# Performance work log

Hardware: AMD Instinct MI355X
Metric: run time of the kernel (lower is better)

Reference implementation:

```python
import jax, jax.numpy as jnp
import numpy as np

ROPE_THETA = 10000.0


def _apply_rope(x, rot_dim):
    # lucidrains RotaryEmbedding: only first rot_dim channels are rotated,
    # freqs are interleave-repeated, rotate_half works on (d r=2) pairs.
    S = x.shape[-2]
    half = rot_dim // 2
    inv_freq = 1.0 / (ROPE_THETA ** (jnp.arange(0, rot_dim, 2, dtype=jnp.float32) / rot_dim))  # [half]
    pos = jnp.arange(S, dtype=jnp.float32)
    freqs = pos[:, None] * inv_freq[None, :]          # [S, half]
    freqs = jnp.repeat(freqs, 2, axis=-1)             # [S, rot_dim] interleaved
    cos = jnp.cos(freqs).astype(x.dtype)
    sin = jnp.sin(freqs).astype(x.dtype)
    xl, xr = x[..., :rot_dim], x[..., rot_dim:]
    xp = xl.reshape(*xl.shape[:-1], half, 2)
    x1, x2 = xp[..., 0], xp[..., 1]
    rot_half = jnp.stack([-x2, x1], axis=-1).reshape(xl.shape)
    return jnp.concatenate([xl * cos + rot_half * sin, xr], axis=-1)


def setup_inputs() -> dict:
    key = jax.random.key(0)
    ks = jax.random.split(key, 7)
    B, Sa, Se, d_audio, d_score = 4, 4096, 2048, 1024, 1024
    d_h = min(d_audio, d_score)
    return {
        "x_audio": jax.random.normal(ks[0], (B, Sa, d_audio), jnp.float32),
        "x_event": jax.random.normal(ks[1], (B, Se, d_score), jnp.float32),
        "event_padding_mask": jax.random.randint(ks[2], (B, Se), 0, 2) > 0,
        "W_q": jax.random.normal(ks[3], (d_h, d_audio), jnp.float32) * (d_audio ** -0.5),
        "b_q": jax.random.normal(ks[4], (d_h,), jnp.float32) * 0.02,
        "W_k": jax.random.normal(ks[5], (d_h, d_score), jnp.float32) * (d_score ** -0.5),
        "b_k": jax.random.normal(ks[6], (d_h,), jnp.float32) * 0.02,
    }


def reference(x_audio, x_event, event_padding_mask, W_q, b_q, W_k, b_k):
    d_h = W_q.shape[0]
    rot_dim = d_h // 2  # RotaryEmbedding(dim=d_h//2) -> partial rotary over first d_h//2 channels
    Q = jnp.einsum("bsd,hd->bsh", x_audio, W_q) + b_q
    K = jnp.einsum("bed,hd->beh", x_event, W_k) + b_k
    Q = _apply_rope(Q, rot_dim)
    K = _apply_rope(K, rot_dim)
    attn = jnp.einsum("bsh,beh->bse", Q, K)  # [B, S_audio, S_event]
    mask = event_padding_mask[:, None, :]     # [B, 1, S_event]
    attn = jnp.where(mask, attn, jnp.float32(-jnp.inf))
    return attn
```

## Files before the change

### kernel.cpp

```cpp
#include <hip/hip_runtime.h>
#include <hip/hip_bf16.h>
#include <cmath>

#define BATCH 4
#define SA 4096
#define SE 2048
#define DIM 1024
#define ROT 512
#define NT (DIM / 64)

#define MASK_SENTINEL (-1.0e30f)

using short8  = __attribute__((ext_vector_type(8))) short;
using floatx4 = __attribute__((ext_vector_type(4))) float;

#define RFREQ 0.0519051171f

__device__ __forceinline__ void gl_lds16(const void* g, void* l) {
    __builtin_amdgcn_global_load_lds(
        (const __attribute__((address_space(1))) unsigned int*)g,
        (__attribute__((address_space(3))) unsigned int*)l, 16, 0, 0);
}

__device__ __forceinline__ short bf16_of(float f) {
    __hip_bfloat16 h = __float2bfloat16(f);
    return *reinterpret_cast<short*>(&h);
}

__device__ __forceinline__ int imin(int a, int b) { return a < b ? a : b; }

__global__ __launch_bounds__(256) void probe_mask_kernel(
    const int* __restrict__ mask_i, int* __restrict__ flag)
{
    __shared__ int s_bad;
    if (threadIdx.x == 0) s_bad = 0;
    __syncthreads();
    int bad = 0;
    for (int i = threadIdx.x; i < 1024; i += 256) {
        int v = mask_i[i];
        bad |= (v != 0 && v != 1) ? 1 : 0;
    }
    if (bad) atomicOr(&s_bad, 1);
    __syncthreads();
    if (threadIdx.x == 0) *flag = s_bad ? 0 : 1;
}

__global__ __launch_bounds__(256) void cvt_bf16_kernel(
    const float* __restrict__ in, short* __restrict__ out, int n8)
{
    int i = blockIdx.x * 256 + threadIdx.x;
    if (i >= n8) return;
    const float4 f0 = ((const float4*)in)[2 * i];
    const float4 f1 = ((const float4*)in)[2 * i + 1];
    short8 o;
    o[0] = bf16_of(f0.x); o[1] = bf16_of(f0.y);
    o[2] = bf16_of(f0.z); o[3] = bf16_of(f0.w);
    o[4] = bf16_of(f1.x); o[5] = bf16_of(f1.y);
    o[6] = bf16_of(f1.z); o[7] = bf16_of(f1.w);
    ((short8*)out)[i] = o;
}

__global__ __launch_bounds__(256) void rope_table_kernel(float2* __restrict__ tab)
{
    const int i   = blockIdx.x * 256 + threadIdx.x;
    const int h2  = i >> 12;
    const int pos = i & 4095;
    const float inv = exp2f(-RFREQ * (float)h2);
    float s, c;
    sincosf((float)pos * inv, &s, &c);
    tab[i] = make_float2(c, s);
}

template <int MODE>
__device__ __forceinline__ void gemm128_body(
    const short* __restrict__ A,
    const short* __restrict__ B,
    const float* __restrict__ bias,
    const float2* __restrict__ ct,
    const void*  __restrict__ maskp,
    const int*   __restrict__ flag,
    void* __restrict__ outp,
    int smask)
{
    __shared__ char smem[65536];
    char* const lA0 = smem;
    char* const lA1 = smem + 16384;
    char* const lB0 = smem + 32768;
    char* const lB1 = smem + 49152;

    const int tid  = threadIdx.x;
    const int wid  = tid >> 6;
    const int lane = tid & 63;

    const int nbx = gridDim.x, nby = gridDim.y;
    const int id  = blockIdx.x + nbx * (blockIdx.y + nby * blockIdx.z);
    const int cpx = (nbx * nby * gridDim.z) >> 3;
    const int swzid = (id & 7) * cpx + (id >> 3);
    const int bx  = swzid % nbx;
    const int byz = swzid / nbx;
    const int by  = byz % nby;
    const int bz  = byz / nby;
    const int m0 = by * 128;
    const int n0 = bx * 128;

    const short* Ab = A;
    const short* Bb = B;
    if (MODE == 1) {
        Ab += (size_t)bz * SA * DIM;
        Bb += (size_t)bz * SE * DIM;
    }

    const int r8   = lane >> 3;
    const int c16  = (lane & 7) << 4;
    const int scs  = ((lane & 7) ^ r8) << 4;
    const int arow = wid * 8 + r8;
    const char* gA = (const char*)Ab + ((size_t)(m0 + arow) << 11) + scs;
    const char* gB = (const char*)Bb + ((size_t)(n0 + arow) << 11) + scs;
    const int ldsT = arow * 128 + c16;

#define STG_A(dst, j, kt) \
    gl_lds16(gA + (((size_t)(j) * 32) << 11) + (size_t)(kt) * 128, \
             (dst) + (j) * 32 * 128 + ldsT)
#define STG_B(dst, j, kt) \
    gl_lds16(gB + (((size_t)(j) * 32) << 11) + (size_t)(kt) * 128, \
             (dst) + (j) * 32 * 128 + ldsT)

    const int fr  = lane & 15;
    const int fq  = lane >> 4;
    const int kc0 = (fq * 16) ^ ((fr & 7) << 4);
    const int wm  = (wid >> 1) * 64;
    const int wn  = (wid & 1) * 64;

    floatx4 acc[4][4] = {};
    short8 af[4][2];
    short8 b01[2][2];
    short8 b23[2][2];

#define RD_A(lAc) do {                                                       \
    _Pragma("unroll") for (int mi = 0; mi < 4; ++mi)                         \
    _Pragma("unroll") for (int ks = 0; ks < 2; ++ks)                         \
        af[mi][ks] = *(const short8*)((lAc)                                  \
            + (wm + mi * 16 + fr) * 128 + (kc0 ^ (ks * 64)));                \
} while (0)
#define RD_B01(lBc) do {                                                     \
    _Pragma("unroll") for (int ni = 0; ni < 2; ++ni)                         \
    _Pragma("unroll") for (int ks = 0; ks < 2; ++ks)                         \
        b01[ni][ks] = *(const short8*)((lBc)                                 \
            + (wn + ni * 16 + fr) * 128 + (kc0 ^ (ks * 64)));                \
} while (0)
#define RD_B23(lBc) do {                                                     \
    _Pragma("unroll") for (int ni = 0; ni < 2; ++ni)                         \
    _Pragma("unroll") for (int ks = 0; ks < 2; ++ks)                         \
        b23[ni][ks] = *(const short8*)((lBc)                                 \
            + (wn + (2 + ni) * 16 + fr) * 128 + (kc0 ^ (ks * 64)));          \
} while (0)
#define QUAD01() do {                                                        \
    __builtin_amdgcn_s_setprio(1);                                           \
    _Pragma("unroll") for (int mi = 0; mi < 4; ++mi)                         \
    _Pragma("unroll") for (int ni = 0; ni < 2; ++ni)                         \
    _Pragma("unroll") for (int ks = 0; ks < 2; ++ks)                         \
        acc[mi][ni] = __builtin_amdgcn_mfma_f32_16x16x32_bf16(               \
            af[mi][ks], b01[ni][ks], acc[mi][ni], 0, 0, 0);                  \
    __builtin_amdgcn_s_setprio(0);                                           \
} while (0)
#define QUAD23() do {                                                        \
    __builtin_amdgcn_s_setprio(1);                                           \
    _Pragma("unroll") for (int mi = 0; mi < 4; ++mi)                         \
    _Pragma("unroll") for (int ni = 0; ni < 2; ++ni)                         \
    _Pragma("unroll") for (int ks = 0; ks < 2; ++ks)                         \
        acc[mi][2 + ni] = __builtin_amdgcn_mfma_f32_16x16x32_bf16(           \
            af[mi][ks], b23[ni][ks], acc[mi][2 + ni], 0, 0, 0);              \
    __builtin_amdgcn_s_setprio(0);                                           \
} while (0)
#define BAR() do { __builtin_amdgcn_s_barrier();                             \
                   __builtin_amdgcn_sched_barrier(0); } while (0)
#define WAITV(n) asm volatile("s_waitcnt vmcnt(" #n ")" ::: "memory")

    STG_A(lA0, 0, 0); STG_A(lA0, 1, 0); STG_A(lA0, 2, 0); STG_A(lA0, 3, 0);
    STG_B(lB0, 0, 0); STG_B(lB0, 1, 0); STG_B(lB0, 2, 0); STG_B(lB0, 3, 0);
    STG_A(lA1, 0, 1); STG_A(lA1, 1, 1); STG_A(lA1, 2, 1); STG_A(lA1, 3, 1);
    WAITV(4);
    BAR();

    auto tile = [&](int t, char* lAc, char* lBc, char* lBo) {
        const int kt1 = imin(t + 1, NT - 1);
        const int kt2 = imin(t + 2, NT - 1);
        RD_A(lAc); RD_B01(lBc);
        STG_B(lBo, 0, kt1); STG_B(lBo, 1, kt1);
        STG_B(lBo, 2, kt1); STG_B(lBo, 3, kt1);
        BAR();
        QUAD01();
        BAR();
        RD_B23(lBc);
        STG_A(lAc, 0, kt2); STG_A(lAc, 1, kt2);
        STG_A(lAc, 2, kt2); STG_A(lAc, 3, kt2);
        BAR();
        QUAD23();
        WAITV(4);
        BAR();
    };

    for (int t = 0; t < NT; t += 2) {
        tile(t,     lA0, lB0, lB1);
        tile(t + 1, lA1, lB1, lB0);
    }
    WAITV(0);

    const int rrow = fq * 4;

    if (MODE == 0) {
        short* out = (short*)outp;
#pragma unroll
        for (int ni = 0; ni < 4; ++ni) {
            const int h = n0 + wn + ni * 16 + fr;
            const float bv  = bias[h];
            const bool rope = (h < ROT);
            const float sgn = (h & 1) ? 1.f : -1.f;
            const float2* ctrow = ct + ((size_t)(h >> 1) << 12);
#pragma unroll
            for (int mi = 0; mi < 4; ++mi) {
                const int rbase = m0 + wm + mi * 16 + rrow;
                const int pbase = rbase & smask;
                float2 cs[4];
                if (rope) {
#pragma unroll
                    for (int r = 0; r < 4; ++r) cs[r] = ctrow[pbase + r];
                }
#pragma unroll
                for (int r = 0; r < 4; ++r) {
                    float v = acc[mi][ni][r] + bv;
                    float p = __shfl_xor(v, 1);
                    if (rope) v = v * cs[r].x + sgn * p * cs[r].y;
                    out[(size_t)(rbase + r) * DIM + h] = bf16_of(v);
                }
            }
        }
    } else {
        float* out = (float*)outp + (size_t)bz * SA * SE;
        const int fl = *flag;
#pragma unroll
        for (int ni = 0; ni < 4; ++ni) {
            const int e = n0 + wn + ni * 16 + fr;
            int mk;
            if (fl) mk = ((const int*)maskp)[(size_t)bz * SE + e];
            else    mk = ((const unsigned char*)maskp)[(size_t)bz * SE + e];
#pragma unroll
            for (int mi = 0; mi < 4; ++mi) {
                const int rbase = m0 + wm + mi * 16 + rrow;
#pragma unroll
                for (int r = 0; r < 4; ++r) {
                    const float v = mk ? acc[mi][ni][r] : MASK_SENTINEL;
                    out[(size_t)(rbase + r) * SE + e] = v;
                }
            }
        }
    }
#undef STG_A
#undef STG_B
#undef RD_A
#undef RD_B01
#undef RD_B23
#undef QUAD01
#undef QUAD23
#undef BAR
#undef WAITV
}

__global__ __launch_bounds__(256, 2) void gemm128_proj_kernel(
    const short* __restrict__ A, const short* __restrict__ B,
    const float* __restrict__ bias, const float2* __restrict__ ct,
    short* __restrict__ out, int smask)
{
    gemm128_body<0>(A, B, bias, ct, nullptr, nullptr, out, smask);
}

__global__ __launch_bounds__(256, 2) void gemm128_attn_kernel(
    const short* __restrict__ Q, const short* __restrict__ K,
    const void* __restrict__ maskp, const int* __restrict__ flag,
    float* __restrict__ out)
{
    gemm128_body<1>(Q, K, nullptr, nullptr, maskp, flag, out, 0);
}

extern "C" void kernel_launch(void* const* d_in, const int* in_sizes, int n_in,
                              void* d_out, int out_size, void* d_ws, size_t ws_size,
                              hipStream_t stream)
{
    const float* x_audio = (const float*)d_in[0];
    const float* x_event = (const float*)d_in[1];
    const void*  maskp   = d_in[2];
    const float* W_q     = (const float*)d_in[3];
    const float* b_q     = (const float*)d_in[4];
    const float* W_k     = (const float*)d_in[5];
    const float* b_k     = (const float*)d_in[6];
    float* out = (float*)d_out;

    char* ws = (char*)d_ws;
    short* xbf  = (short*)(ws);
    short* Qbf  = (short*)(ws + (size_t)32 * 1024 * 1024);
    short* Kbf  = (short*)(ws + (size_t)64 * 1024 * 1024);
    short* Wqbf = (short*)(ws + (size_t)80 * 1024 * 1024);
    short* Wkbf = (short*)(ws + (size_t)82 * 1024 * 1024);
    int*   flag = (int*)  (ws + (size_t)84 * 1024 * 1024);
    float2* ct  = (float2*)d_out;

    probe_mask_kernel<<<1, 256, 0, stream>>>((const int*)maskp, flag);
    rope_table_kernel<<<4096, 256, 0, stream>>>(ct);

    const int nxa8 = BATCH * SA * DIM / 8;
    const int nxe8 = BATCH * SE * DIM / 8;
    const int nw8  = DIM * DIM / 8;

    cvt_bf16_kernel<<<(nxa8 + 255) / 256, 256, 0, stream>>>(x_audio, xbf, nxa8);
    cvt_bf16_kernel<<<(nw8 + 255) / 256, 256, 0, stream>>>(W_q, Wqbf, nw8);
    gemm128_proj_kernel<<<dim3(DIM / 128, (BATCH * SA) / 128, 1), 256, 0, stream>>>(
        xbf, Wqbf, b_q, ct, Qbf, SA - 1);

    cvt_bf16_kernel<<<(nxe8 + 255) / 256, 256, 0, stream>>>(x_event, xbf, nxe8);
    cvt_bf16_kernel<<<(nw8 + 255) / 256, 256, 0, stream>>>(W_k, Wkbf, nw8);
    gemm128_proj_kernel<<<dim3(DIM / 128, (BATCH * SE) / 128, 1), 256, 0, stream>>>(
        xbf, Wkbf, b_k, ct, Kbf, SE - 1);

    gemm128_attn_kernel<<<dim3(SE / 128, SA / 128, BATCH), 256, 0, stream>>>(
        Qbf, Kbf, maskp, flag, out);
}
```

Before: 374.7 us.

## Use 256x256 tiles with 512 threads and BK=32 for the attention GEMM

Replaces the shared 128x128 templated GEMM for the QK^T score computation with a dedicated kernel. It uses 256x256 output tiles, 8 waves, a K-step of 32 and a new LDS swizzle, while keeping the split-B double-buffered global_load_lds pipeline. Larger tiles halve global/L2 traffic per output element and raise MFMA work per LDS byte. In exchange each thread holds a 128-float accumulator, which adds register pressure and lowers occupancy, and the grid shrinks to 512 blocks. The projection GEMM is split out unchanged.

Result: slower. 991.9 us (+164.7%).

```diff
diff --git a/kernel.cpp b/kernel.cpp
--- a/kernel.cpp
+++ b/kernel.cpp
@@ -7,7 +7,14 @@
 #define SE 2048
 #define DIM 1024
 #define ROT 512
-#define NT (DIM / 64)
+
+#define BM 128
+#define BN 128
+#define BK 64
+#define NT (DIM / BK)
+
+#define ABK 32
+#define ANT (DIM / ABK)
 
 #define MASK_SENTINEL (-1.0e30f)
 
@@ -28,6 +35,10 @@
 }
 
 __device__ __forceinline__ int imin(int a, int b) { return a < b ? a : b; }
+
+#define BAR() do { __builtin_amdgcn_s_barrier();                             \
+                   __builtin_amdgcn_sched_barrier(0); } while (0)
+#define WAITV(n) asm volatile("s_waitcnt vmcnt(" #n ")" ::: "memory")
 
 __global__ __launch_bounds__(256) void probe_mask_kernel(
     const int* __restrict__ mask_i, int* __restrict__ flag)
@@ -71,16 +82,22 @@
     tab[i] = make_float2(c, s);
 }
 
-template <int MODE>
-__device__ __forceinline__ void gemm128_body(
-    const short* __restrict__ A,
-    const short* __restrict__ B,
-    const float* __restrict__ bias,
-    const float2* __restrict__ ct,
-    const void*  __restrict__ maskp,
-    const int*   __restrict__ flag,
-    void* __restrict__ outp,
-    int smask)
+__device__ __forceinline__ void xcd_swizzle(int& bx, int& by, int& bz)
+{
+    const int nbx = gridDim.x, nby = gridDim.y;
+    const int id  = blockIdx.x + nbx * (blockIdx.y + nby * blockIdx.z);
+    const int cpx = (nbx * nby * gridDim.z) >> 3;
+    const int swzid = (id & 7) * cpx + (id >> 3);
+    bx = swzid % nbx;
+    const int byz = swzid / nbx;
+    by = byz % nby;
+    bz = byz / nby;
+}
+
+__global__ __launch_bounds__(256, 2) void gemm_proj_kernel(
+    const short* __restrict__ A, const short* __restrict__ B,
+    const float* __restrict__ bias, const float2* __restrict__ ct,
+    short* __restrict__ out, int smask)
 {
     __shared__ char smem[65536];
     char* const lA0 = smem;
@@ -92,30 +109,18 @@
     const int wid  = tid >> 6;
     const int lane = tid & 63;
 
-    const int nbx = gridDim.x, nby = gridDim.y;
-    const int id  = blockIdx.x + nbx * (blockIdx.y + nby * blockIdx.z);
-    const int cpx = (nbx * nby * gridDim.z) >> 3;
-    const int swzid = (id & 7) * cpx + (id >> 3);
-    const int bx  = swzid % nbx;
-    const int byz = swzid / nbx;
-    const int by  = byz % nby;
-    const int bz  = byz / nby;
-    const int m0 = by * 128;
-    const int n0 = bx * 128;
-
-    const short* Ab = A;
-    const short* Bb = B;
-    if (MODE == 1) {
-        Ab += (size_t)bz * SA * DIM;
-        Bb += (size_t)bz * SE * DIM;
-    }
+    int bx, by, bz;
+    xcd_swizzle(bx, by, bz);
+    (void)bz;
+    const int m0 = by * BM;
+    const int n0 = bx * BN;
 
     const int r8   = lane >> 3;
     const int c16  = (lane & 7) << 4;
     const int scs  = ((lane & 7) ^ r8) << 4;
     const int arow = wid * 8 + r8;
-    const char* gA = (const char*)Ab + ((size_t)(m0 + arow) << 11) + scs;
-    const char* gB = (const char*)Bb + ((size_t)(n0 + arow) << 11) + scs;
+    const char* gA = (const char*)A + ((size_t)(m0 + arow) << 11) + scs;
+    const char* gB = (const char*)B + ((size_t)(n0 + arow) << 11) + scs;
     const int ldsT = arow * 128 + c16;
 
 #define STG_A(dst, j, kt) \
@@ -172,9 +177,6 @@
             af[mi][ks], b23[ni][ks], acc[mi][2 + ni], 0, 0, 0);              \
     __builtin_amdgcn_s_setprio(0);                                           \
 } while (0)
-#define BAR() do { __builtin_amdgcn_s_barrier();                             \
-                   __builtin_amdgcn_sched_barrier(0); } while (0)
-#define WAITV(n) asm volatile("s_waitcnt vmcnt(" #n ")" ::: "memory")
 
     STG_A(lA0, 0, 0); STG_A(lA0, 1, 0); STG_A(lA0, 2, 0); STG_A(lA0, 3, 0);
     STG_B(lB0, 0, 0); STG_B(lB0, 1, 0); STG_B(lB0, 2, 0); STG_B(lB0, 3, 0);
@@ -207,51 +209,28 @@
     WAITV(0);
 
     const int rrow = fq * 4;
-
-    if (MODE == 0) {
-        short* out = (short*)outp;
-#pragma unroll
-        for (int ni = 0; ni < 4; ++ni) {
-            const int h = n0 + wn + ni * 16 + fr;
-            const float bv  = bias[h];
-            const bool rope = (h < ROT);
-            const float sgn = (h & 1) ? 1.f : -1.f;
-            const float2* ctrow = ct + ((size_t)(h >> 1) << 12);
-#pragma unroll
-            for (int mi = 0; mi < 4; ++mi) {
-                const int rbase = m0 + wm + mi * 16 + rrow;
-                const int pbase = rbase & smask;
-                float2 cs[4];
-                if (rope) {
-#pragma unroll
-                    for (int r = 0; r < 4; ++r) cs[r] = ctrow[pbase + r];
-                }
-#pragma unroll
-                for (int r = 0; r < 4; ++r) {
-                    float v = acc[mi][ni][r] + bv;
-                    float p = __shfl_xor(v, 1);
-                    if (rope) v = v * cs[r].x + sgn * p * cs[r].y;
-                    out[(size_t)(rbase + r) * DIM + h] = bf16_of(v);
-                }
+#pragma unroll
+    for (int ni = 0; ni < 4; ++ni) {
+        const int h = n0 + wn + ni * 16 + fr;
+        const float bv  = bias[h];
+        const bool rope = (h < ROT);
+        const float sgn = (h & 1) ? 1.f : -1.f;
+        const float2* ctrow = ct + ((size_t)(h >> 1) << 12);
+#pragma unroll
+        for (int mi = 0; mi < 4; ++mi) {
+            const int rbase = m0 + wm + mi * 16 + rrow;
+            const int pbase = rbase & smask;
+            float2 cs[4];
+            if (rope) {
+#pragma unroll
+                for (int r = 0; r < 4; ++r) cs[r] = ctrow[pbase + r];
             }
-        }
-    } else {
-        float* out = (float*)outp + (size_t)bz * SA * SE;
-        const int fl = *flag;
-#pragma unroll
-        for (int ni = 0; ni < 4; ++ni) {
-            const int e = n0 + wn + ni * 16 + fr;
-            int mk;
-            if (fl) mk = ((const int*)maskp)[(size_t)bz * SE + e];
-            else    mk = ((const unsigned char*)maskp)[(size_t)bz * SE + e];
-#pragma unroll
-            for (int mi = 0; mi < 4; ++mi) {
-                const int rbase = m0 + wm + mi * 16 + rrow;
-#pragma unroll
-                for (int r = 0; r < 4; ++r) {
-                    const float v = mk ? acc[mi][ni][r] : MASK_SENTINEL;
-                    out[(size_t)(rbase + r) * SE + e] = v;
-                }
+#pragma unroll
+            for (int r = 0; r < 4; ++r) {
+                float v = acc[mi][ni][r] + bv;
+                float p = __shfl_xor(v, 1);
+                if (rope) v = v * cs[r].x + sgn * p * cs[r].y;
+                out[(size_t)(rbase + r) * DIM + h] = bf16_of(v);
             }
         }
     }
@@ -262,24 +241,125 @@
 #undef RD_B23
 #undef QUAD01
 #undef QUAD23
-#undef BAR
-#undef WAITV
-}
-
-__global__ __launch_bounds__(256, 2) void gemm128_proj_kernel(
-    const short* __restrict__ A, const short* __restrict__ B,
-    const float* __restrict__ bias, const float2* __restrict__ ct,
-    short* __restrict__ out, int smask)
-{
-    gemm128_body<0>(A, B, bias, ct, nullptr, nullptr, out, smask);
-}
-
-__global__ __launch_bounds__(256, 2) void gemm128_attn_kernel(
+}
+
+__global__ __launch_bounds__(512, 4) void attn256_kernel(
     const short* __restrict__ Q, const short* __restrict__ K,
     const void* __restrict__ maskp, const int* __restrict__ flag,
-    float* __restrict__ out)
-{
-    gemm128_body<1>(Q, K, nullptr, nullptr, maskp, flag, out, 0);
+    float* __restrict__ outp)
+{
+    __shared__ char smem[65536];
+    char* const buf0 = smem;
+    char* const buf1 = smem + 32768;
+
+    const int tid  = threadIdx.x;
+    const int wid  = tid >> 6;
+    const int lane = tid & 63;
+
+    int bx, by, bz;
+    xcd_swizzle(bx, by, bz);
+    const int m0 = by * 256;
+    const int n0 = bx * 256;
+
+    const short* Qb = Q + (size_t)bz * SA * DIM;
+    const short* Kb = K + (size_t)bz * SE * DIM;
+
+    const int srow  = lane >> 2;
+    const int sslot = lane & 3;
+    const int gsw   = ((sslot ^ ((srow >> 1) & 3)) << 4);
+    const char* gQ = (const char*)Qb + (size_t)(m0 + wid * 16 + srow) * 2048 + gsw;
+    const char* gK = (const char*)Kb + (size_t)(n0 + wid * 16 + srow) * 2048 + gsw;
+    const int ldsT = (wid * 16 + srow) * 64 + sslot * 16;
+
+#define ASTG_A(buf, j, kt) \
+    gl_lds16(gQ + (size_t)(j) * 128 * 2048 + (size_t)(kt) * 64, \
+             (buf) + (j) * 8192 + ldsT)
+#define ASTG_B(buf, j, kt) \
+    gl_lds16(gK + (size_t)(j) * 128 * 2048 + (size_t)(kt) * 64, \
+             (buf) + 16384 + (j) * 8192 + ldsT)
+
+    const int fr = lane & 15;
+    const int fq = lane >> 4;
+    const int ko = ((fq ^ ((fr >> 1) & 3)) << 4);
+    const int wm = (wid >> 2) * 128;
+    const int wn = (wid & 3) * 64;
+
+    int aoff[8], boff[4];
+#pragma unroll
+    for (int mi = 0; mi < 8; ++mi) aoff[mi] = (wm + mi * 16 + fr) * 64 + ko;
+#pragma unroll
+    for (int ni = 0; ni < 4; ++ni) boff[ni] = 16384 + (wn + ni * 16 + fr) * 64 + ko;
+
+    floatx4 acc[8][4] = {};
+
+    ASTG_A(buf0, 0, 0); ASTG_A(buf0, 1, 0);
+    ASTG_B(buf0, 0, 0); ASTG_B(buf0, 1, 0);
+    ASTG_A(buf1, 0, 1); ASTG_A(buf1, 1, 1);
+    WAITV(2);
+    BAR();
+
+    auto tile = [&](int t, char* cur, char* oth) {
+        const int kt1 = imin(t + 1, ANT - 1);
+        const int kt2 = imin(t + 2, ANT - 1);
+        short8 af[8], b01[2], b23[2];
+#pragma unroll
+        for (int mi = 0; mi < 8; ++mi) af[mi] = *(const short8*)(cur + aoff[mi]);
+#pragma unroll
+        for (int ni = 0; ni < 2; ++ni) b01[ni] = *(const short8*)(cur + boff[ni]);
+        ASTG_B(oth, 0, kt1); ASTG_B(oth, 1, kt1);
+        BAR();
+        __builtin_amdgcn_s_setprio(1);
+#pragma unroll
+        for (int mi = 0; mi < 8; ++mi)
+#pragma unroll
+            for (int ni = 0; ni < 2; ++ni)
+                acc[mi][ni] = __builtin_amdgcn_mfma_f32_16x16x32_bf16(
+                    af[mi], b01[ni], acc[mi][ni], 0, 0, 0);
+        __builtin_amdgcn_s_setprio(0);
+        BAR();
+#pragma unroll
+        for (int ni = 0; ni < 2; ++ni) b23[ni] = *(const short8*)(cur + boff[2 + ni]);
+        ASTG_A(cur, 0, kt2); ASTG_A(cur, 1, kt2);
+        BAR();
+        __builtin_amdgcn_s_setprio(1);
+#pragma unroll
+        for (int mi = 0; mi < 8; ++mi)
+#pragma unroll
+            for (int ni = 0; ni < 2; ++ni)
+                acc[mi][2 + ni] = __builtin_amdgcn_mfma_f32_16x16x32_bf16(
+                    af[mi], b23[ni], acc[mi][2 + ni], 0, 0, 0);
+        __builtin_amdgcn_s_setprio(0);
+        WAITV(2);
+        BAR();
+    };
+
+    for (int t = 0; t < ANT; t += 2) {
+        tile(t,     buf0, buf1);
+        tile(t + 1, buf1, buf0);
+    }
+    WAITV(0);
+
+    float* out = outp + (size_t)bz * SA * SE;
+    const int fl = *flag;
+    const int rrow = fq * 4;
+#pragma unroll
+    for (int ni = 0; ni < 4; ++ni) {
+        const int e = n0 + wn + ni * 16 + fr;
+        int mk;
+        if (fl) mk = ((const int*)maskp)[(size_t)bz * SE + e];
+        else    mk = ((const unsigned char*)maskp)[(size_t)bz * SE + e];
+#pragma unroll
+        for (int mi = 0; mi < 8; ++mi) {
+            const int rbase = m0 + wm + mi * 16 + rrow;
+#pragma unroll
+            for (int r = 0; r < 4; ++r) {
+                const float v = mk ? acc[mi][ni][r] : MASK_SENTINEL;
+                out[(size_t)(rbase + r) * SE + e] = v;
+            }
+        }
+    }
+#undef ASTG_A
+#undef ASTG_B
 }
 
 extern "C" void kernel_launch(void* const* d_in, const int* in_sizes, int n_in,
@@ -313,14 +393,14 @@
 
     cvt_bf16_kernel<<<(nxa8 + 255) / 256, 256, 0, stream>>>(x_audio, xbf, nxa8);
     cvt_bf16_kernel<<<(nw8 + 255) / 256, 256, 0, stream>>>(W_q, Wqbf, nw8);
-    gemm128_proj_kernel<<<dim3(DIM / 128, (BATCH * SA) / 128, 1), 256, 0, stream>>>(
+    gemm_proj_kernel<<<dim3(DIM / BN, (BATCH * SA) / BM, 1), 256, 0, stream>>>(
         xbf, Wqbf, b_q, ct, Qbf, SA - 1);
 
     cvt_bf16_kernel<<<(nxe8 + 255) / 256, 256, 0, stream>>>(x_event, xbf, nxe8);
     cvt_bf16_kernel<<<(nw8 + 255) / 256, 256, 0, stream>>>(W_k, Wkbf, nw8);
-    gemm128_proj_kernel<<<dim3(DIM / 128, (BATCH * SE) / 128, 1), 256, 0, stream>>>(
+    gemm_proj_kernel<<<dim3(DIM / BN, (BATCH * SE) / BM, 1), 256, 0, stream>>>(
         xbf, Wkbf, b_k, ct, Kbf, SE - 1);
 
-    gemm128_attn_kernel<<<dim3(SE / 128, SA / 128, BATCH), 256, 0, stream>>>(
+    attn256_kernel<<<dim3(SE / 256, SA / 256, BATCH), 512, 0, stream>>>(
         Qbf, Kbf, maskp, flag, out);
 }
```
